# Optimization experiments

Measured on AMD Instinct MI355X. Metric: run time of the kernel, lower is better.

Reference implementation:

```python
import jax, jax.numpy as jnp
import numpy as np

P, G = 8192, 4096
SH_DEG = 2            # active_sh_degree = max_sh_degree = 2 -> 9 SH coeffs
N_SH = (SH_DEG + 1) ** 2
C0 = 0.28209479177387814
C1 = 0.4886025119029199
C2 = (1.0925484305920792, -1.0925484305920792, 0.31539156525252005,
      -1.0925484305920792, 0.5462742152960396)
CMIN, CMAX = 0.0, 1.0  # config.rendering.coord_min/max


def setup_inputs() -> dict:
    key = jax.random.key(0)
    ks = jax.random.split(key, 7)
    position_rx = jax.random.uniform(ks[0], (P, 3), dtype=jnp.float32)  # in [cmin,cmax]
    mean = jax.random.uniform(ks[1], (G, 3), dtype=jnp.float32) * 2.0 - 1.0
    features_dc = jax.random.uniform(ks[2], (G, 1, 1), dtype=jnp.float32) * 0.2 - 0.1
    features_rest = jax.random.normal(ks[3], (G, 1, N_SH - 1), dtype=jnp.float32) * 0.05
    scaling = jnp.float32(np.log(0.3)) + 0.1 * jax.random.normal(ks[4], (G, 3), dtype=jnp.float32)
    rotation = jax.random.normal(ks[5], (G, 4), dtype=jnp.float32)
    opacity = jax.random.normal(ks[6], (G, 1), dtype=jnp.float32)
    return dict(position_rx=position_rx, mean=mean, features_dc=features_dc,
                features_rest=features_rest, scaling=scaling, rotation=rotation,
                opacity=opacity)


def _quat_to_rot(q):
    # q: [G,4] (w,x,y,z), normalized (rotation_activation = F.normalize)
    q = q / jnp.linalg.norm(q, axis=-1, keepdims=True)
    r, x, y, z = q[:, 0], q[:, 1], q[:, 2], q[:, 3]
    R = jnp.stack([
        jnp.stack([1 - 2 * (y * y + z * z), 2 * (x * y - r * z), 2 * (x * z + r * y)], -1),
        jnp.stack([2 * (x * y + r * z), 1 - 2 * (x * x + z * z), 2 * (y * z - r * x)], -1),
        jnp.stack([2 * (x * z - r * y), 2 * (y * z + r * x), 1 - 2 * (x * x + y * y)], -1),
    ], axis=-2)  # [G,3,3]
    return R


def _eval_sh(sh, dirs):
    # sh: [G, 9]; dirs: [P, G, 3] unit vectors -> [P, G]
    x, y, z = dirs[..., 0], dirs[..., 1], dirs[..., 2]
    res = C0 * sh[:, 0]
    res = (res - C1 * y * sh[:, 1] + C1 * z * sh[:, 2] - C1 * x * sh[:, 3])
    xx, yy, zz = x * x, y * y, z * z
    res = (res
           + C2[0] * (x * y) * sh[:, 4]
           + C2[1] * (y * z) * sh[:, 5]
           + C2[2] * (2.0 * zz - xx - yy) * sh[:, 6]
           + C2[3] * (x * z) * sh[:, 7]
           + C2[4] * (xx - yy) * sh[:, 8])
    return res


def reference(position_rx, mean, features_dc, features_rest, scaling, rotation, opacity):
    # normalize_points: map [cmin,cmax] -> [-1,1]
    q = (position_rx - CMIN) / (CMAX - CMIN) * 2.0 - 1.0  # [P,3]

    # covariance_activation: Sigma = L L^T, L = R diag(s); use precision directly
    scales = jnp.exp(scaling)                    # [G,3]
    inv_var = 1.0 / (scales * scales)            # [G,3]
    R = _quat_to_rot(rotation)                   # [G,3,3]
    Sinv = jnp.einsum('gik,gk,gjk->gij', R, inv_var, R)  # Sigma^{-1} [G,3,3]

    diff = q[:, None, :] - mean[None, :, :]      # [P,G,3]
    mahal = jnp.einsum('pgi,gij,pgj->pg', diff, Sinv, diff)  # [P,G]
    gauss = jnp.exp(-0.5 * mahal)                # [P,G]

    # eval_features: normalized direction point -> gaussian, SH evaluation
    dirs = diff / (jnp.linalg.norm(diff, axis=-1, keepdims=True) + 1e-8)
    sh = jnp.concatenate([features_dc, features_rest], axis=-1)[:, 0, :]  # [G,9]
    feat = _eval_sh(sh, dirs)                    # [P,G]

    alpha = jax.nn.sigmoid(opacity)[:, 0]        # [G]
    out = jnp.einsum('pg,g->p', feat * gauss, alpha)  # splat accumulate
    return out[:, None]                          # [P,1]
```

## Files before the change

### kernel.cpp

```cpp
#include <hip/hip_runtime.h>
#include <hip/hip_bf16.h>

constexpr int P = 8192;
constexpr int G = 4096;
constexpr int BLK = 256;
constexpr int GSPLIT = 128;
constexpr int CHUNK = G / GSPLIT;
constexpr int PPT = 4;
constexpr int PBLK = BLK * PPT;
constexpr float LOG2E = 1.4426950408889634f;

__device__ __forceinline__ float fast_exp2(float x) {
  float r;
  asm("v_exp_f32 %0, %1" : "=v"(r) : "v"(x));
  return r;
}

__global__ __launch_bounds__(BLK) void fused_main(
    const float* __restrict__ pos,
    const float* __restrict__ mean, const float* __restrict__ fdc,
    const float* __restrict__ frest, const float* __restrict__ scal,
    const float* __restrict__ rot, const float* __restrict__ opac,
    float* __restrict__ partial) {
  __shared__ float4 sg[CHUNK * 5];

  const int t = threadIdx.x;
  const int c = blockIdx.y;
  const int pbase = blockIdx.x * PBLK + t;

  float px[PPT], py[PPT], pz[PPT], acc[PPT];
#pragma unroll
  for (int k = 0; k < PPT; ++k) {
    const int p = pbase + k * BLK;
    px[k] = pos[p * 3 + 0] * 2.0f - 1.0f;
    py[k] = pos[p * 3 + 1] * 2.0f - 1.0f;
    pz[k] = pos[p * 3 + 2] * 2.0f - 1.0f;
    acc[k] = 0.0f;
  }

  if (t < CHUNK) {
    const int g = c * CHUNK + t;

    float qr = rot[g * 4 + 0], qx = rot[g * 4 + 1];
    float qy = rot[g * 4 + 2], qz = rot[g * 4 + 3];
    float qn = 1.0f / sqrtf(qr * qr + qx * qx + qy * qy + qz * qz);
    qr *= qn; qx *= qn; qy *= qn; qz *= qn;

    float R00 = 1.f - 2.f * (qy * qy + qz * qz);
    float R01 = 2.f * (qx * qy - qr * qz);
    float R02 = 2.f * (qx * qz + qr * qy);
    float R10 = 2.f * (qx * qy + qr * qz);
    float R11 = 1.f - 2.f * (qx * qx + qz * qz);
    float R12 = 2.f * (qy * qz - qr * qx);
    float R20 = 2.f * (qx * qz - qr * qy);
    float R21 = 2.f * (qy * qz + qr * qx);
    float R22 = 1.f - 2.f * (qx * qx + qy * qy);

    float sc0 = expf(scal[g * 3 + 0]);
    float sc1 = expf(scal[g * 3 + 1]);
    float sc2 = expf(scal[g * 3 + 2]);
    float iv0 = 1.0f / (sc0 * sc0);
    float iv1 = 1.0f / (sc1 * sc1);
    float iv2 = 1.0f / (sc2 * sc2);

    float s00 = R00 * R00 * iv0 + R01 * R01 * iv1 + R02 * R02 * iv2;
    float s11 = R10 * R10 * iv0 + R11 * R11 * iv1 + R12 * R12 * iv2;
    float s22 = R20 * R20 * iv0 + R21 * R21 * iv1 + R22 * R22 * iv2;
    float s01 = R00 * R10 * iv0 + R01 * R11 * iv1 + R02 * R12 * iv2;
    float s02 = R00 * R20 * iv0 + R01 * R21 * iv1 + R02 * R22 * iv2;
    float s12 = R10 * R20 * iv0 + R11 * R21 * iv1 + R12 * R22 * iv2;

    const float kD = -0.5f * LOG2E;
    const float kO = -LOG2E;

    float alpha = 1.0f / (1.0f + expf(-opac[g]));

    const float C0 = 0.28209479177387814f;
    const float C1 = 0.4886025119029199f;
    float a0 = C0 * fdc[g] * alpha;
    float a1 = -C1 * frest[g * 8 + 0] * alpha;
    float a2 =  C1 * frest[g * 8 + 1] * alpha;
    float a3 = -C1 * frest[g * 8 + 2] * alpha;
    float a4 =  1.0925484305920792f  * frest[g * 8 + 3] * alpha;
    float a5 = -1.0925484305920792f  * frest[g * 8 + 4] * alpha;
    float a6 =  0.31539156525252005f * frest[g * 8 + 5] * alpha;
    float a7 = -1.0925484305920792f  * frest[g * 8 + 6] * alpha;
    float a8 =  0.5462742152960396f  * frest[g * 8 + 7] * alpha;

    float mx = mean[g * 3 + 0], my = mean[g * 3 + 1], mz = mean[g * 3 + 2];

    sg[t * 5 + 0] = make_float4(mx, my, mz, kD * s00);
    sg[t * 5 + 1] = make_float4(kD * s11, kD * s22, kO * s01, kO * s02);
    sg[t * 5 + 2] = make_float4(kO * s12, a0, a1, a2);
    sg[t * 5 + 3] = make_float4(a3, a4, a5, a7);
    sg[t * 5 + 4] = make_float4(a8 - a6, -a8 - a6, 2.f * a6, 0.f);
  }

  __syncthreads();

#pragma unroll 2
  for (int gi = 0; gi < CHUNK; ++gi) {
    const float4 v0 = sg[gi * 5 + 0];
    const float4 v1 = sg[gi * 5 + 1];
    const float4 v2 = sg[gi * 5 + 2];
    const float4 v3 = sg[gi * 5 + 3];
    const float4 v4 = sg[gi * 5 + 4];

#pragma unroll
    for (int k = 0; k < PPT; ++k) {
      const float dx = px[k] - v0.x, dy = py[k] - v0.y, dz = pz[k] - v0.z;
      const float dxx = dx * dx, dyy = dy * dy, dzz = dz * dz;
      const float dxdy = dx * dy, dxdz = dx * dz, dydz = dy * dz;
      const float d2 = dxx + dyy + dzz;

      float m = v0.w * dxx;
      m = fmaf(v1.x, dyy, m);
      m = fmaf(v1.y, dzz, m);
      m = fmaf(v1.z, dxdy, m);
      m = fmaf(v1.w, dxdz, m);
      m = fmaf(v2.x, dydz, m);
      const float gauss = fast_exp2(m);

      const float inv = __builtin_amdgcn_rsqf(fmaxf(d2, 1e-16f));
      const float inv2 = inv * inv;

      float lin = v2.z * dy;
      lin = fmaf(v2.w, dz, lin);
      lin = fmaf(v3.x, dx, lin);

      float quad = v3.y * dxdy;
      quad = fmaf(v3.z, dydz, quad);
      quad = fmaf(v3.w, dxdz, quad);
      quad = fmaf(v4.x, dxx, quad);
      quad = fmaf(v4.y, dyy, quad);
      quad = fmaf(v4.z, dzz, quad);

      float feat = fmaf(inv, lin, v2.y);
      feat = fmaf(inv2, quad, feat);

      acc[k] = fmaf(gauss, feat, acc[k]);
    }
  }

#pragma unroll
  for (int k = 0; k < PPT; ++k) {
    partial[(size_t)c * P + pbase + k * BLK] = acc[k];
  }
}

__global__ __launch_bounds__(256) void reduce_kernel(
    const float* __restrict__ partial, float* __restrict__ out) {
  __shared__ float red[4][64];
  const int t = threadIdx.x;
  const int lane = t & 63;
  const int s = t >> 6;
  const int p = blockIdx.x * 64 + lane;
  const int cbase = s * 32;

  float a0 = 0.f, a1 = 0.f, a2 = 0.f, a3 = 0.f;
#pragma unroll
  for (int j = 0; j < 32; j += 4) {
    a0 += partial[(size_t)(cbase + j + 0) * P + p];
    a1 += partial[(size_t)(cbase + j + 1) * P + p];
    a2 += partial[(size_t)(cbase + j + 2) * P + p];
    a3 += partial[(size_t)(cbase + j + 3) * P + p];
  }
  red[s][lane] = (a0 + a1) + (a2 + a3);
  __syncthreads();

  if (t < 64) {
    out[p] = (red[0][lane] + red[1][lane]) + (red[2][lane] + red[3][lane]);
  }
}

extern "C" void kernel_launch(void* const* d_in, const int* in_sizes, int n_in,
                              void* d_out, int out_size, void* d_ws, size_t ws_size,
                              hipStream_t stream) {
  const float* pos   = (const float*)d_in[0];
  const float* mean  = (const float*)d_in[1];
  const float* fdc   = (const float*)d_in[2];
  const float* frest = (const float*)d_in[3];
  const float* scal  = (const float*)d_in[4];
  const float* rot   = (const float*)d_in[5];
  const float* opac  = (const float*)d_in[6];
  float* out = (float*)d_out;

  float* partial = (float*)d_ws;

  fused_main<<<dim3(P / PBLK, GSPLIT), BLK, 0, stream>>>(
      pos, mean, fdc, frest, scal, rot, opac, partial);
  reduce_kernel<<<P / 64, 256, 0, stream>>>(partial, out);
}
```

Measured before the change: 34.69 us.

## Split gaussian precompute into separate kernel and stream params via scalar loads

Moves the per-gaussian covariance/SH/opacity precomputation out of the main kernel into a dedicated precompute kernel that writes packed float4 parameters to workspace. The main kernel then reads the uniform per-gaussian parameters through inline-asm scalar (SMEM) loads instead of LDS, removing the shared memory staging, the __syncthreads barrier, and the redundant recomputation across the 8 point-blocks per chunk. This adds an extra kernel launch and a workspace round trip, and each iteration now waits on lgkmcnt(0) for the scalar loads, which may expose scalar-cache latency in the inner loop.

```diff
diff --git a/kernel.cpp b/kernel.cpp
--- a/kernel.cpp
+++ b/kernel.cpp
@@ -10,23 +10,85 @@
 constexpr int PBLK = BLK * PPT;
 constexpr float LOG2E = 1.4426950408889634f;
 
+typedef float sf4 __attribute__((ext_vector_type(4)));
+
 __device__ __forceinline__ float fast_exp2(float x) {
   float r;
   asm("v_exp_f32 %0, %1" : "=v"(r) : "v"(x));
   return r;
 }
 
-__global__ __launch_bounds__(BLK) void fused_main(
-    const float* __restrict__ pos,
+__global__ __launch_bounds__(256) void precomp_kernel(
     const float* __restrict__ mean, const float* __restrict__ fdc,
     const float* __restrict__ frest, const float* __restrict__ scal,
     const float* __restrict__ rot, const float* __restrict__ opac,
+    float4* __restrict__ pre) {
+  int g = blockIdx.x * blockDim.x + threadIdx.x;
+  if (g >= G) return;
+
+  float qr = rot[g * 4 + 0], qx = rot[g * 4 + 1];
+  float qy = rot[g * 4 + 2], qz = rot[g * 4 + 3];
+  float qn = 1.0f / sqrtf(qr * qr + qx * qx + qy * qy + qz * qz);
+  qr *= qn; qx *= qn; qy *= qn; qz *= qn;
+
+  float R00 = 1.f - 2.f * (qy * qy + qz * qz);
+  float R01 = 2.f * (qx * qy - qr * qz);
+  float R02 = 2.f * (qx * qz + qr * qy);
+  float R10 = 2.f * (qx * qy + qr * qz);
+  float R11 = 1.f - 2.f * (qx * qx + qz * qz);
+  float R12 = 2.f * (qy * qz - qr * qx);
+  float R20 = 2.f * (qx * qz - qr * qy);
+  float R21 = 2.f * (qy * qz + qr * qx);
+  float R22 = 1.f - 2.f * (qx * qx + qy * qy);
+
+  float sc0 = expf(scal[g * 3 + 0]);
+  float sc1 = expf(scal[g * 3 + 1]);
+  float sc2 = expf(scal[g * 3 + 2]);
+  float iv0 = 1.0f / (sc0 * sc0);
+  float iv1 = 1.0f / (sc1 * sc1);
+  float iv2 = 1.0f / (sc2 * sc2);
+
+  float s00 = R00 * R00 * iv0 + R01 * R01 * iv1 + R02 * R02 * iv2;
+  float s11 = R10 * R10 * iv0 + R11 * R11 * iv1 + R12 * R12 * iv2;
+  float s22 = R20 * R20 * iv0 + R21 * R21 * iv1 + R22 * R22 * iv2;
+  float s01 = R00 * R10 * iv0 + R01 * R11 * iv1 + R02 * R12 * iv2;
+  float s02 = R00 * R20 * iv0 + R01 * R21 * iv1 + R02 * R22 * iv2;
+  float s12 = R10 * R20 * iv0 + R11 * R21 * iv1 + R12 * R22 * iv2;
+
+  const float kD = -0.5f * LOG2E;
+  const float kO = -LOG2E;
+
+  float alpha = 1.0f / (1.0f + expf(-opac[g]));
+
+  const float C0 = 0.28209479177387814f;
+  const float C1 = 0.4886025119029199f;
+  float a0 = C0 * fdc[g] * alpha;
+  float a1 = -C1 * frest[g * 8 + 0] * alpha;
+  float a2 =  C1 * frest[g * 8 + 1] * alpha;
+  float a3 = -C1 * frest[g * 8 + 2] * alpha;
+  float a4 =  1.0925484305920792f  * frest[g * 8 + 3] * alpha;
+  float a5 = -1.0925484305920792f  * frest[g * 8 + 4] * alpha;
+  float a6 =  0.31539156525252005f * frest[g * 8 + 5] * alpha;
+  float a7 = -1.0925484305920792f  * frest[g * 8 + 6] * alpha;
+  float a8 =  0.5462742152960396f  * frest[g * 8 + 7] * alpha;
+
+  float mx = mean[g * 3 + 0], my = mean[g * 3 + 1], mz = mean[g * 3 + 2];
+
+  pre[g * 5 + 0] = make_float4(mx, my, mz, kD * s00);
+  pre[g * 5 + 1] = make_float4(kD * s11, kD * s22, kO * s01, kO * s02);
+  pre[g * 5 + 2] = make_float4(kO * s12, a0, a1, a2);
+  pre[g * 5 + 3] = make_float4(a3, a4, a5, a7);
+  pre[g * 5 + 4] = make_float4(a8 - a6, -a8 - a6, 2.f * a6, 0.f);
+}
+
+__global__ __launch_bounds__(BLK) void main_kernel(
+    const float* __restrict__ pos, const float* __restrict__ pre,
     float* __restrict__ partial) {
-  __shared__ float4 sg[CHUNK * 5];
-
   const int t = threadIdx.x;
   const int c = blockIdx.y;
   const int pbase = blockIdx.x * PBLK + t;
+
+  const float* __restrict__ gbase = pre + (size_t)c * CHUNK * 20;
 
   float px[PPT], py[PPT], pz[PPT], acc[PPT];
 #pragma unroll
@@ -38,104 +100,50 @@
     acc[k] = 0.0f;
   }
 
-  if (t < CHUNK) {
-    const int g = c * CHUNK + t;
-
-    float qr = rot[g * 4 + 0], qx = rot[g * 4 + 1];
-    float qy = rot[g * 4 + 2], qz = rot[g * 4 + 3];
-    float qn = 1.0f / sqrtf(qr * qr + qx * qx + qy * qy + qz * qz);
-    qr *= qn; qx *= qn; qy *= qn; qz *= qn;
-
-    float R00 = 1.f - 2.f * (qy * qy + qz * qz);
-    float R01 = 2.f * (qx * qy - qr * qz);
-    float R02 = 2.f * (qx * qz + qr * qy);
-    float R10 = 2.f * (qx * qy + qr * qz);
-    float R11 = 1.f - 2.f * (qx * qx + qz * qz);
-    float R12 = 2.f * (qy * qz - qr * qx);
-    float R20 = 2.f * (qx * qz - qr * qy);
-    float R21 = 2.f * (qy * qz + qr * qx);
-    float R22 = 1.f - 2.f * (qx * qx + qy * qy);
-
-    float sc0 = expf(scal[g * 3 + 0]);
-    float sc1 = expf(scal[g * 3 + 1]);
-    float sc2 = expf(scal[g * 3 + 2]);
-    float iv0 = 1.0f / (sc0 * sc0);
-    float iv1 = 1.0f / (sc1 * sc1);
-    float iv2 = 1.0f / (sc2 * sc2);
-
-    float s00 = R00 * R00 * iv0 + R01 * R01 * iv1 + R02 * R02 * iv2;
-    float s11 = R10 * R10 * iv0 + R11 * R11 * iv1 + R12 * R12 * iv2;
-    float s22 = R20 * R20 * iv0 + R21 * R21 * iv1 + R22 * R22 * iv2;
-    float s01 = R00 * R10 * iv0 + R01 * R11 * iv1 + R02 * R12 * iv2;
-    float s02 = R00 * R20 * iv0 + R01 * R21 * iv1 + R02 * R22 * iv2;
-    float s12 = R10 * R20 * iv0 + R11 * R21 * iv1 + R12 * R22 * iv2;
-
-    const float kD = -0.5f * LOG2E;
-    const float kO = -LOG2E;
-
-    float alpha = 1.0f / (1.0f + expf(-opac[g]));
-
-    const float C0 = 0.28209479177387814f;
-    const float C1 = 0.4886025119029199f;
-    float a0 = C0 * fdc[g] * alpha;
-    float a1 = -C1 * frest[g * 8 + 0] * alpha;
-    float a2 =  C1 * frest[g * 8 + 1] * alpha;
-    float a3 = -C1 * frest[g * 8 + 2] * alpha;
-    float a4 =  1.0925484305920792f  * frest[g * 8 + 3] * alpha;
-    float a5 = -1.0925484305920792f  * frest[g * 8 + 4] * alpha;
-    float a6 =  0.31539156525252005f * frest[g * 8 + 5] * alpha;
-    float a7 = -1.0925484305920792f  * frest[g * 8 + 6] * alpha;
-    float a8 =  0.5462742152960396f  * frest[g * 8 + 7] * alpha;
-
-    float mx = mean[g * 3 + 0], my = mean[g * 3 + 1], mz = mean[g * 3 + 2];
-
-    sg[t * 5 + 0] = make_float4(mx, my, mz, kD * s00);
-    sg[t * 5 + 1] = make_float4(kD * s11, kD * s22, kO * s01, kO * s02);
-    sg[t * 5 + 2] = make_float4(kO * s12, a0, a1, a2);
-    sg[t * 5 + 3] = make_float4(a3, a4, a5, a7);
-    sg[t * 5 + 4] = make_float4(a8 - a6, -a8 - a6, 2.f * a6, 0.f);
-  }
-
-  __syncthreads();
-
 #pragma unroll 2
   for (int gi = 0; gi < CHUNK; ++gi) {
-    const float4 v0 = sg[gi * 5 + 0];
-    const float4 v1 = sg[gi * 5 + 1];
-    const float4 v2 = sg[gi * 5 + 2];
-    const float4 v3 = sg[gi * 5 + 3];
-    const float4 v4 = sg[gi * 5 + 4];
+    sf4 b0, b1, b2, b3, b4;
+    const float* ga = gbase + gi * 20;
+    asm volatile(
+        "s_load_dwordx4 %0, %5, 0x0\n\t"
+        "s_load_dwordx4 %1, %5, 0x10\n\t"
+        "s_load_dwordx4 %2, %5, 0x20\n\t"
+        "s_load_dwordx4 %3, %5, 0x30\n\t"
+        "s_load_dwordx4 %4, %5, 0x40\n\t"
+        "s_waitcnt lgkmcnt(0)"
+        : "=&s"(b0), "=&s"(b1), "=&s"(b2), "=&s"(b3), "=&s"(b4)
+        : "s"(ga));
 
 #pragma unroll
     for (int k = 0; k < PPT; ++k) {
-      const float dx = px[k] - v0.x, dy = py[k] - v0.y, dz = pz[k] - v0.z;
+      const float dx = px[k] - b0.x, dy = py[k] - b0.y, dz = pz[k] - b0.z;
       const float dxx = dx * dx, dyy = dy * dy, dzz = dz * dz;
       const float dxdy = dx * dy, dxdz = dx * dz, dydz = dy * dz;
       const float d2 = dxx + dyy + dzz;
 
-      float m = v0.w * dxx;
-      m = fmaf(v1.x, dyy, m);
-      m = fmaf(v1.y, dzz, m);
-      m = fmaf(v1.z, dxdy, m);
-      m = fmaf(v1.w, dxdz, m);
-      m = fmaf(v2.x, dydz, m);
+      float m = b0.w * dxx;
+      m = fmaf(b1.x, dyy, m);
+      m = fmaf(b1.y, dzz, m);
+      m = fmaf(b1.z, dxdy, m);
+      m = fmaf(b1.w, dxdz, m);
+      m = fmaf(b2.x, dydz, m);
       const float gauss = fast_exp2(m);
 
       const float inv = __builtin_amdgcn_rsqf(fmaxf(d2, 1e-16f));
       const float inv2 = inv * inv;
 
-      float lin = v2.z * dy;
-      lin = fmaf(v2.w, dz, lin);
-      lin = fmaf(v3.x, dx, lin);
-
-      float quad = v3.y * dxdy;
-      quad = fmaf(v3.z, dydz, quad);
-      quad = fmaf(v3.w, dxdz, quad);
-      quad = fmaf(v4.x, dxx, quad);
-      quad = fmaf(v4.y, dyy, quad);
-      quad = fmaf(v4.z, dzz, quad);
-
-      float feat = fmaf(inv, lin, v2.y);
+      float lin = b2.z * dy;
+      lin = fmaf(b2.w, dz, lin);
+      lin = fmaf(b3.x, dx, lin);
+
+      float quad = b3.y * dxdy;
+      quad = fmaf(b3.z, dydz, quad);
+      quad = fmaf(b3.w, dxdz, quad);
+      quad = fmaf(b4.x, dxx, quad);
+      quad = fmaf(b4.y, dyy, quad);
+      quad = fmaf(b4.z, dzz, quad);
+
+      float feat = fmaf(inv, lin, b2.y);
       feat = fmaf(inv2, quad, feat);
 
       acc[k] = fmaf(gauss, feat, acc[k]);
@@ -185,9 +193,10 @@
   const float* opac  = (const float*)d_in[6];
   float* out = (float*)d_out;
 
-  float* partial = (float*)d_ws;
-
-  fused_main<<<dim3(P / PBLK, GSPLIT), BLK, 0, stream>>>(
-      pos, mean, fdc, frest, scal, rot, opac, partial);
+  float4* pre = (float4*)d_ws;
+  float* partial = (float*)((char*)d_ws + (size_t)G * 5 * sizeof(float4));
+
+  precomp_kernel<<<G / 256, 256, 0, stream>>>(mean, fdc, frest, scal, rot, opac, pre);
+  main_kernel<<<dim3(P / PBLK, GSPLIT), BLK, 0, stream>>>(pos, (const float*)pre, partial);
   reduce_kernel<<<P / 64, 256, 0, stream>>>(partial, out);
 }
```

Result: slower. 46.69 us (+34.6%).
